# Kernel optimization log

Measured on AMD Instinct MI355X. Metric: run time of the kernel, lower is better.

## Reference

```python
import jax, jax.numpy as jnp
import numpy as np

DT_MIN, DT_MAX = 1e-3, 0.1
DT_RANK, D_STATE = 64, 16


def setup_inputs() -> dict:
    key = jax.random.key(0)
    ks = jax.random.split(key, 8)
    B, L, D_MODEL, D_INNER = 2, 4096, 1024, 2048
    s = 0.02
    return {
        "x": jax.random.normal(ks[0], (B, L, D_MODEL), jnp.float32),
        "W_in": jax.random.normal(ks[1], (D_MODEL, 2 * D_INNER), jnp.float32) * s,
        "W_xproj": jax.random.normal(ks[2], (D_INNER, DT_RANK + 2 * D_STATE), jnp.float32) * s,
        "W_dt": jax.random.normal(ks[3], (DT_RANK, D_INNER), jnp.float32) * s,
        "b_dt": jax.random.normal(ks[4], (D_INNER,), jnp.float32) * s,
        "A_log": jnp.log(jax.random.uniform(ks[5], (D_INNER, D_STATE), jnp.float32) + 0.5),
        "D": jnp.ones((D_INNER,), jnp.float32),
        "W_out": jax.random.normal(ks[6], (D_INNER, D_MODEL), jnp.float32) * s,
    }


def _selective_scan(xp, delta, A, Bm, Cm):
    # xp, delta: [B, L, d_inner]; Bm, Cm: [B, L, d_state]; A: [d_inner, d_state]
    batch, L, d_inner = xp.shape
    d_state = A.shape[1]

    def step(h, inp):
        x_t, dt_t, B_t, C_t = inp  # [B,di], [B,di], [B,ds], [B,ds]
        A_bar = 1.0 + A[None] * dt_t[..., None]            # [B, di, ds]
        B_bar = B_t[:, None, :] * dt_t[..., None]          # [B, di, ds]
        h = A_bar * h + B_bar * x_t[..., None]             # [B, di, ds]
        y_t = jnp.sum(C_t[:, None, :] * h, axis=-1)        # [B, di]
        return h, y_t

    h0 = jnp.zeros((batch, d_inner, d_state), xp.dtype)
    xs = (
        jnp.swapaxes(xp, 0, 1),
        jnp.swapaxes(delta, 0, 1),
        jnp.swapaxes(Bm, 0, 1),
        jnp.swapaxes(Cm, 0, 1),
    )
    _, ys = jax.lax.scan(step, h0, xs)  # ys: [L, B, d_inner]
    return jnp.swapaxes(ys, 0, 1)


def reference(x, W_in, W_xproj, W_dt, b_dt, A_log, D, W_out):
    xz = x @ W_in
    xp, z = jnp.split(xz, 2, axis=-1)                      # [B,L,d_inner] each
    x_dbl = xp @ W_xproj
    dlt, Bm, Cm = jnp.split(x_dbl, [DT_RANK, DT_RANK + D_STATE], axis=-1)
    delta = jnp.clip(jax.nn.softplus(dlt @ W_dt + b_dt), DT_MIN, DT_MAX)
    A = -jnp.exp(A_log)
    y = _selective_scan(xp, delta, A, Bm, Cm)
    y = y + D[None, None, :] * xp
    y = y * jax.nn.silu(z)
    return y @ W_out
```

## Files before the change

kernel.cpp:

```cpp
#include <hip/hip_runtime.h>
#include <cstdint>
#include <cstddef>

typedef unsigned short u16;
typedef __attribute__((ext_vector_type(8))) short bf16x8;
typedef __attribute__((ext_vector_type(4))) float f32x4;

__device__ __forceinline__ float bf2f(u16 u) {
  unsigned v = ((unsigned)u) << 16;
  return __builtin_bit_cast(float, v);
}
__device__ __forceinline__ u16 f2bf(float f) {
  unsigned u = __builtin_bit_cast(unsigned, f);
  u = (u + 0x7FFFu + ((u >> 16) & 1u)) >> 16;
  return (u16)u;
}

__device__ __forceinline__ void gload16(const void* g, void* l) {
  __builtin_amdgcn_global_load_lds(
      (const __attribute__((address_space(1))) void*)g,
      (__attribute__((address_space(3))) void*)l,
      16, 0, 0);
}

__device__ __forceinline__ int swz(int lb) { return lb ^ (((lb >> 7) & 7) << 4); }

__global__ __launch_bounds__(256) void f32_to_bf16_kernel(
    const float* __restrict__ in, u16* __restrict__ out, int n) {
  int i = (blockIdx.x * 256 + threadIdx.x) * 4;
  if (i < n) {
    float4 v = *(const float4*)(in + i);
    ushort4 o;
    o.x = f2bf(v.x); o.y = f2bf(v.y); o.z = f2bf(v.z); o.w = f2bf(v.w);
    *(ushort4*)(out + i) = o;
  }
}

__global__ void transpose_f32_bf16T_kernel(
    const float* __restrict__ in, u16* __restrict__ out, int R, int C) {
  __shared__ float tile[32][33];
  const int bx = blockIdx.x * 32;
  const int by = blockIdx.y * 32;
  const int tx = threadIdx.x, ty = threadIdx.y;
#pragma unroll
  for (int i = 0; i < 32; i += 8)
    tile[ty + i][tx] = in[(size_t)(by + ty + i) * C + bx + tx];
  __syncthreads();
#pragma unroll
  for (int i = 0; i < 32; i += 8)
    out[(size_t)(bx + ty + i) * R + by + tx] = f2bf(tile[tx][ty + i]);
}

template <int BN, int EPI>
__global__ __launch_bounds__(512, 2) void gemm256(
    const u16* __restrict__ Ap, const u16* __restrict__ Btp,
    int M, int N, int K, int gx,
    void* __restrict__ o0, void* __restrict__ o1) {
  constexpr int NFR = BN / 64;
  constexpr int NFH = NFR / 2;
  constexpr int B_ISS = BN / 64;
  constexpr int BH = B_ISS / 2;
  constexpr int WN = BN / 4;
  constexpr int HSH = (BN == 256) ? 5 : 4;
  constexpr int AREG = 32768;
  constexpr int BREG = BN * 128;
  __shared__ __align__(1024) char smem[AREG + BREG];

  const int tid = threadIdx.x;
  const int wid = tid >> 6, lane = tid & 63;
  const int wr = wid >> 2, wc = wid & 3;
  const int l16 = lane & 15, lk = lane >> 4;

  const int nwg = gridDim.x, bid = blockIdx.x;
  const int rb = (bid & 7) * (nwg >> 3) + (bid >> 3);
  const int bx = rb % gx, by = rb / gx;
  const int m0 = by * 256, n0 = bx * BN;

  const u16* gA[4];
  const u16* gB[B_ISS];
#pragma unroll
  for (int i = 0; i < 4; ++i) {
    int lb = swz(i * 8192 + tid * 16);
    gA[i] = Ap + (size_t)(m0 + (lb >> 7)) * K + ((lb & 127) >> 1);
  }
#pragma unroll
  for (int i = 0; i < B_ISS; ++i) {
    int lb = swz(i * 8192 + tid * 16);
    int rl = lb >> 7;
    int half = (rl >= BN / 2) ? 1 : 0;
    int r = rl & (BN / 2 - 1);
    int n = ((r >> HSH) << (HSH + 1)) + (half << HSH) + (r & ((1 << HSH) - 1));
    gB[i] = Btp + (size_t)(n0 + n) * K + ((lb & 127) >> 1);
  }

  auto stageA = [&](int kt, int h) {
    char* dst = smem + (wid << 10);
    gload16(gA[h] + kt * 64, dst + h * 8192);
    gload16(gA[h + 2] + kt * 64, dst + (h + 2) * 8192);
  };
  auto stageB = [&](int kt, int h) {
    char* dst = smem + AREG + (wid << 10);
#pragma unroll
    for (int j = 0; j < BH; ++j)
      gload16(gB[h * BH + j] + kt * 64, dst + (h * BH + j) * 8192);
  };

  auto offA = [&](int f, int kk) {
    return swz((wr * 128 + f * 16 + l16) * 128 + kk * 64 + lk * 16);
  };
  auto offB = [&](int nf, int kk) {
    int rl = (nf >= NFH ? BN / 2 : 0) + wc * (WN / 2) + (nf % NFH) * 16 + l16;
    return swz(rl * 128 + kk * 64 + lk * 16);
  };

  f32x4 acc[8][NFR];
#pragma unroll
  for (int f = 0; f < 8; ++f)
#pragma unroll
    for (int n = 0; n < NFR; ++n) {
      f32x4 z = {0.f, 0.f, 0.f, 0.f};
      acc[f][n] = z;
    }

  const char* bufA = smem;
  const char* bufB = smem + AREG;
  const int NT = K >> 6;
  stageA(0, 0); stageB(0, 0); stageB(0, 1); stageA(0, 1);
  if constexpr (BH == 2) asm volatile("s_waitcnt vmcnt(4)" ::: "memory");
  else                   asm volatile("s_waitcnt vmcnt(3)" ::: "memory");
  __builtin_amdgcn_s_barrier();

  for (int kt = 0; kt < NT; ++kt) {
    bf16x8 af[4][2], bh[2][NFH][2];

#pragma unroll
    for (int j = 0; j < 4; ++j)
#pragma unroll
      for (int kk = 0; kk < 2; ++kk)
        af[j][kk] = *(const bf16x8*)(bufA + offA(j, kk));
#pragma unroll
    for (int j = 0; j < NFH; ++j)
#pragma unroll
      for (int kk = 0; kk < 2; ++kk)
        bh[0][j][kk] = *(const bf16x8*)(bufB + offB(j, kk));
    __builtin_amdgcn_s_barrier();
    asm volatile("s_waitcnt lgkmcnt(0)" ::: "memory");
    __builtin_amdgcn_sched_barrier(0);
    __builtin_amdgcn_s_setprio(1);
#pragma unroll
    for (int j = 0; j < 4; ++j)
#pragma unroll
      for (int n2 = 0; n2 < NFH; ++n2)
#pragma unroll
        for (int kk = 0; kk < 2; ++kk)
          acc[j][n2] = __builtin_amdgcn_mfma_f32_16x16x32_bf16(
              af[j][kk], bh[0][n2][kk], acc[j][n2], 0, 0, 0);
    __builtin_amdgcn_s_setprio(0);
    asm volatile("s_waitcnt vmcnt(2)" ::: "memory");
    __builtin_amdgcn_s_barrier();

#pragma unroll
    for (int j = 0; j < NFH; ++j)
#pragma unroll
      for (int kk = 0; kk < 2; ++kk)
        bh[1][j][kk] = *(const bf16x8*)(bufB + offB(NFH + j, kk));
    if (kt + 1 < NT) { stageA(kt + 1, 0); stageB(kt + 1, 0); }
    __builtin_amdgcn_s_barrier();
    asm volatile("s_waitcnt lgkmcnt(0)" ::: "memory");
    __builtin_amdgcn_sched_barrier(0);
    __builtin_amdgcn_s_setprio(1);
#pragma unroll
    for (int j = 0; j < 4; ++j)
#pragma unroll
      for (int n2 = 0; n2 < NFH; ++n2)
#pragma unroll
        for (int kk = 0; kk < 2; ++kk)
          acc[j][NFH + n2] = __builtin_amdgcn_mfma_f32_16x16x32_bf16(
              af[j][kk], bh[1][n2][kk], acc[j][NFH + n2], 0, 0, 0);
    __builtin_amdgcn_s_setprio(0);
    if (kt + 1 < NT) {
      if constexpr (BH == 2) asm volatile("s_waitcnt vmcnt(4)" ::: "memory");
      else                   asm volatile("s_waitcnt vmcnt(3)" ::: "memory");
    } else {
      asm volatile("s_waitcnt vmcnt(0)" ::: "memory");
    }
    __builtin_amdgcn_s_barrier();

#pragma unroll
    for (int j = 0; j < 4; ++j)
#pragma unroll
      for (int kk = 0; kk < 2; ++kk)
        af[j][kk] = *(const bf16x8*)(bufA + offA(4 + j, kk));
    if (kt + 1 < NT) stageB(kt + 1, 1);
    __builtin_amdgcn_s_barrier();
    asm volatile("s_waitcnt lgkmcnt(0)" ::: "memory");
    __builtin_amdgcn_sched_barrier(0);
    __builtin_amdgcn_s_setprio(1);
#pragma unroll
    for (int j = 0; j < 4; ++j)
#pragma unroll
      for (int n2 = 0; n2 < NFH; ++n2)
#pragma unroll
        for (int kk = 0; kk < 2; ++kk)
          acc[4 + j][NFH + n2] = __builtin_amdgcn_mfma_f32_16x16x32_bf16(
              af[j][kk], bh[1][n2][kk], acc[4 + j][NFH + n2], 0, 0, 0);
    __builtin_amdgcn_s_setprio(0);
    __builtin_amdgcn_s_barrier();

    if (kt + 1 < NT) stageA(kt + 1, 1);
    __builtin_amdgcn_s_setprio(1);
#pragma unroll
    for (int j = 0; j < 4; ++j)
#pragma unroll
      for (int n2 = 0; n2 < NFH; ++n2)
#pragma unroll
        for (int kk = 0; kk < 2; ++kk)
          acc[4 + j][n2] = __builtin_amdgcn_mfma_f32_16x16x32_bf16(
              af[j][kk], bh[0][n2][kk], acc[4 + j][n2], 0, 0, 0);
    __builtin_amdgcn_s_setprio(0);
    if (kt + 1 < NT) {
      if constexpr (BH == 2) asm volatile("s_waitcnt vmcnt(4)" ::: "memory");
      else                   asm volatile("s_waitcnt vmcnt(3)" ::: "memory");
    }
    __builtin_amdgcn_s_barrier();
  }

#pragma unroll
  for (int f = 0; f < 8; ++f) {
#pragma unroll
    for (int n = 0; n < NFR; ++n) {
#pragma unroll
      for (int rr = 0; rr < 4; ++rr) {
        const int row = m0 + wr * 128 + f * 16 + lk * 4 + rr;
        const int col = n0 + wc * WN + n * 16 + l16;
        float v = acc[f][n][rr];
        if constexpr (EPI == 0) {
          if (col < 2048) {
            ((u16*)o0)[(size_t)row * 2048 + col] = f2bf(v);
          } else {
            float sv = v / (1.f + __expf(-v));
            ((u16*)o1)[(size_t)row * 2048 + (col - 2048)] = f2bf(sv);
          }
        } else {
          ((float*)o0)[(size_t)row * (size_t)N + col] = v;
        }
      }
    }
  }
}

template <int BN, int NR, int EPI>
__global__ __launch_bounds__(256) void gemm_bt(
    const u16* __restrict__ A, const u16* __restrict__ Bt,
    int M, int N, int K, int KS,
    void* __restrict__ o0, const float* __restrict__ bias) {
  constexpr int BM = 128, BK = 32, MR = 4;
  __shared__ __align__(16) u16 As[BM * BK];
  __shared__ __align__(16) u16 Bs[BN * BK];
  const int tid = threadIdx.x;
  const int wid = tid >> 6, lane = tid & 63;
  const int wr = wid >> 1, wc = wid & 1;
  const int m0 = blockIdx.y * BM, n0 = blockIdx.x * BN;
  const int l16 = lane & 15, lk = lane >> 4;

  f32x4 acc[MR][NR];
#pragma unroll
  for (int m = 0; m < MR; ++m)
#pragma unroll
    for (int n = 0; n < NR; ++n) {
      f32x4 z = {0.f, 0.f, 0.f, 0.f};
      acc[m][n] = z;
    }

  constexpr int CH_A = (BM * BK * 2) / 1024;
  constexpr int CH_B = (BN * BK * 2) / 1024;

  const int kbeg = blockIdx.z * KS, kend = kbeg + KS;
  for (int k0 = kbeg; k0 < kend; k0 += BK) {
    for (int c = wid; c < CH_A; c += 4) {
      int off = c * 1024 + lane * 16;
      int e = off >> 1;
      int m = e >> 5, kk = e & 31;
      gload16(A + (size_t)(m0 + m) * K + (k0 + kk), (char*)As + off);
    }
    for (int c = wid; c < CH_B; c += 4) {
      int off = c * 1024 + lane * 16;
      int e = off >> 1;
      int n = e >> 5, kk = e & 31;
      gload16(Bt + (size_t)(n0 + n) * K + (k0 + kk), (char*)Bs + off);
    }
    __syncthreads();
    bf16x8 af[MR], bfr[NR];
#pragma unroll
    for (int m = 0; m < MR; ++m)
      af[m] = *(const bf16x8*)(As + (wr * 64 + m * 16 + l16) * BK + lk * 8);
#pragma unroll
    for (int n = 0; n < NR; ++n)
      bfr[n] = *(const bf16x8*)(Bs + (wc * (NR * 16) + n * 16 + l16) * BK + lk * 8);
#pragma unroll
    for (int m = 0; m < MR; ++m)
#pragma unroll
      for (int n = 0; n < NR; ++n)
        acc[m][n] = __builtin_amdgcn_mfma_f32_16x16x32_bf16(af[m], bfr[n], acc[m][n], 0, 0, 0);
    __syncthreads();
  }

#pragma unroll
  for (int m = 0; m < MR; ++m) {
#pragma unroll
    for (int n = 0; n < NR; ++n) {
#pragma unroll
      for (int r = 0; r < 4; ++r) {
        const int row = m0 + wr * 64 + m * 16 + (lane >> 4) * 4 + r;
        const int col = n0 + wc * (NR * 16) + n * 16 + (lane & 15);
        float v = acc[m][n][r];
        if constexpr (EPI == 2) {
          v += bias[col];
          float sp = (v > 20.f) ? v : log1pf(__expf(v));
          sp = fminf(fmaxf(sp, 1e-3f), 0.1f);
          ((u16*)o0)[(size_t)row * 2048 + col] = f2bf(sp);
        } else {
          ((float*)o0)[((size_t)blockIdx.z * M + row) * 96 + col] = v;
        }
      }
    }
  }
}

__global__ __launch_bounds__(256) void reduce_xdbl(
    const float* __restrict__ part, u16* __restrict__ dlt,
    float* __restrict__ Bc, float* __restrict__ Cc) {
  int idx = blockIdx.x * 256 + threadIdx.x;
  int row = idx / 24, c4 = idx % 24;
  const float* p = part + (size_t)row * 96 + c4 * 4;
  f32x4 v = *(const f32x4*)p;
#pragma unroll
  for (int z = 1; z < 4; ++z)
    v += *(const f32x4*)(p + (size_t)z * 8192 * 96);
  int col = c4 * 4;
  if (col < 64) {
    ushort4 o;
    o.x = f2bf(v[0]); o.y = f2bf(v[1]); o.z = f2bf(v[2]); o.w = f2bf(v[3]);
    *(ushort4*)(dlt + (size_t)row * 64 + col) = o;
  } else if (col < 80) {
    *(f32x4*)(Bc + (size_t)row * 16 + (col - 64)) = v;
  } else {
    *(f32x4*)(Cc + (size_t)row * 16 + (col - 80)) = v;
  }
}

template <int TC>
__global__ __launch_bounds__(256) void scan_pass1(
    const u16* __restrict__ xp, const u16* __restrict__ dt,
    const float* __restrict__ Bc, const float* __restrict__ A_log,
    float* __restrict__ P, float* __restrict__ Q, int NC) {
  const int di = blockIdx.x * 256 + threadIdx.x;
  const int c = blockIdx.y, b = blockIdx.z;
  __shared__ __align__(16) float Bs[TC * 16];
  {
    const float* src = Bc + (size_t)(b * 4096 + c * TC) * 16;
    for (int i = threadIdx.x; i < TC * 4; i += 256)
      *(float4*)(Bs + i * 4) = *(const float4*)(src + i * 4);
  }
  float A[16], h[16], Pp[16];
#pragma unroll
  for (int s = 0; s < 16; ++s) {
    A[s] = -__expf(A_log[di * 16 + s]);
    h[s] = 0.f;
    Pp[s] = 1.f;
  }
  __syncthreads();
  size_t gidx = (size_t)(b * 4096 + c * TC) * 2048 + di;
  for (int t = 0; t < TC; ++t, gidx += 2048) {
    float xv = bf2f(xp[gidx]), dv = bf2f(dt[gidx]);
    float dvx = dv * xv;
#pragma unroll
    for (int q = 0; q < 4; ++q) {
      f32x4 bv = ((const f32x4*)(Bs + t * 16))[q];
#pragma unroll
      for (int j = 0; j < 4; ++j) {
        int s = q * 4 + j;
        float abar = fmaf(A[s], dv, 1.f);
        h[s] = fmaf(abar, h[s], bv[j] * dvx);
        Pp[s] *= abar;
      }
    }
  }
  const size_t obase = ((size_t)(b * NC + c) * 16) * 2048 + di;
#pragma unroll
  for (int s = 0; s < 16; ++s) {
    P[obase + (size_t)s * 2048] = Pp[s];
    Q[obase + (size_t)s * 2048] = h[s];
  }
}

__global__ __launch_bounds__(256) void scan_pass2(
    const float* __restrict__ P, const float* __restrict__ Q,
    float* __restrict__ Hin, int NC) {
  const int di = blockIdx.x * 256 + threadIdx.x;
  const int s = blockIdx.y, b = blockIdx.z;
  float hin = 0.f;
  const size_t idx0 = ((size_t)(b * NC) * 16 + s) * 2048 + di;
#pragma unroll 8
  for (int c = 0; c < NC; ++c) {
    size_t idx = idx0 + (size_t)c * (16 * 2048);
    Hin[idx] = hin;
    hin = fmaf(P[idx], hin, Q[idx]);
  }
}

template <int TC>
__global__ __launch_bounds__(256) void scan_pass3(
    const u16* __restrict__ xp, const u16* __restrict__ dt,
    const u16* __restrict__ zs, const float* __restrict__ Bc,
    const float* __restrict__ Cc, const float* __restrict__ A_log,
    const float* __restrict__ Dv, const float* __restrict__ Hin,
    u16* __restrict__ Y, int NC) {
  const int di = blockIdx.x * 256 + threadIdx.x;
  const int c = blockIdx.y, b = blockIdx.z;
  __shared__ __align__(16) float Bs[TC * 16], Cs[TC * 16];
  {
    const float* srcB = Bc + (size_t)(b * 4096 + c * TC) * 16;
    const float* srcC = Cc + (size_t)(b * 4096 + c * TC) * 16;
    for (int i = threadIdx.x; i < TC * 4; i += 256) {
      *(float4*)(Bs + i * 4) = *(const float4*)(srcB + i * 4);
      *(float4*)(Cs + i * 4) = *(const float4*)(srcC + i * 4);
    }
  }
  float A[16], h[16];
  const size_t hbase = ((size_t)(b * NC + c) * 16) * 2048 + di;
#pragma unroll
  for (int s = 0; s < 16; ++s) {
    A[s] = -__expf(A_log[di * 16 + s]);
    h[s] = Hin[hbase + (size_t)s * 2048];
  }
  const float Dg = Dv[di];
  __syncthreads();
  size_t gidx = (size_t)(b * 4096 + c * TC) * 2048 + di;
  for (int t = 0; t < TC; ++t, gidx += 2048) {
    float xv = bf2f(xp[gidx]), dv = bf2f(dt[gidx]), zv = bf2f(zs[gidx]);
    float dvx = dv * xv;
    float y = 0.f;
#pragma unroll
    for (int q = 0; q < 4; ++q) {
      f32x4 bv = ((const f32x4*)(Bs + t * 16))[q];
      f32x4 cv = ((const f32x4*)(Cs + t * 16))[q];
#pragma unroll
      for (int j = 0; j < 4; ++j) {
        int s = q * 4 + j;
        float abar = fmaf(A[s], dv, 1.f);
        h[s] = fmaf(abar, h[s], bv[j] * dvx);
        y = fmaf(cv[j], h[s], y);
      }
    }
    float yo = fmaf(Dg, xv, y) * zv;
    Y[gidx] = f2bf(yo);
  }
}

extern "C" void kernel_launch(void* const* d_in, const int* in_sizes, int n_in,
                              void* d_out, int out_size, void* d_ws, size_t ws_size,
                              hipStream_t stream) {
  (void)in_sizes; (void)n_in; (void)out_size; (void)ws_size;
  const float* x       = (const float*)d_in[0];
  const float* W_in    = (const float*)d_in[1];
  const float* W_xproj = (const float*)d_in[2];
  const float* W_dt    = (const float*)d_in[3];
  const float* b_dt    = (const float*)d_in[4];
  const float* A_log   = (const float*)d_in[5];
  const float* Dv      = (const float*)d_in[6];
  const float* W_out   = (const float*)d_in[7];
  float* out = (float*)d_out;

  constexpr size_t MB = 1ull << 20;
  char* ws = (char*)d_ws;
  constexpr size_t O_XP    = 0;
  constexpr size_t O_ZS    = 32 * MB;
  constexpr size_t O_DELTA = 64 * MB;
  constexpr size_t O_BC    = 96 * MB;
  constexpr size_t O_CC    = O_BC + 512 * 1024;
  constexpr size_t O_WOUTT = 97 * MB;
  constexpr size_t O_Y     = 101 * MB;
  constexpr size_t O_XB    = 133 * MB;
  constexpr size_t O_WINT  = 149 * MB;
  constexpr size_t O_WXT   = 157 * MB;
  constexpr size_t O_WDTT  = O_WXT + 393216;
  constexpr size_t O_DLT   = O_WDTT + 262144;
  constexpr size_t O_P     = 133 * MB;
  constexpr size_t O_Q     = 149 * MB;
  constexpr size_t O_HIN   = 165 * MB;
  constexpr size_t O_XDP   = O_P;

  u16* xb    = (u16*)(ws + O_XB);
  u16* WinT  = (u16*)(ws + O_WINT);
  u16* WxT   = (u16*)(ws + O_WXT);
  u16* WdtT  = (u16*)(ws + O_WDTT);
  u16* WoutT = (u16*)(ws + O_WOUTT);
  u16* xpb   = (u16*)(ws + O_XP);
  u16* zsb   = (u16*)(ws + O_ZS);
  u16* dltb  = (u16*)(ws + O_DLT);
  float* Bcf = (float*)(ws + O_BC);
  float* Ccf = (float*)(ws + O_CC);
  u16* delb  = (u16*)(ws + O_DELTA);
  u16* Yb    = (u16*)(ws + O_Y);
  float* Pf  = (float*)(ws + O_P);
  float* Qf  = (float*)(ws + O_Q);
  float* Hin = (float*)(ws + O_HIN);
  float* xdp = (float*)(ws + O_XDP);

  dim3 tb(32, 8);
  f32_to_bf16_kernel<<<8192 * 1024 / 1024, 256, 0, stream>>>(x, xb, 8192 * 1024);
  transpose_f32_bf16T_kernel<<<dim3(4096 / 32, 1024 / 32), tb, 0, stream>>>(W_in, WinT, 1024, 4096);
  transpose_f32_bf16T_kernel<<<dim3(96 / 32, 2048 / 32), tb, 0, stream>>>(W_xproj, WxT, 2048, 96);
  transpose_f32_bf16T_kernel<<<dim3(2048 / 32, 64 / 32), tb, 0, stream>>>(W_dt, WdtT, 64, 2048);
  transpose_f32_bf16T_kernel<<<dim3(1024 / 32, 2048 / 32), tb, 0, stream>>>(W_out, WoutT, 2048, 1024);

  gemm256<256, 0><<<512, 512, 0, stream>>>(
      xb, WinT, 8192, 4096, 1024, 16, xpb, zsb);
  gemm_bt<96, 3, 4><<<dim3(1, 8192 / 128, 4), 256, 0, stream>>>(
      xpb, WxT, 8192, 96, 2048, 512, xdp, nullptr);
  reduce_xdbl<<<8192 * 24 / 256, 256, 0, stream>>>(xdp, dltb, Bcf, Ccf);
  gemm_bt<128, 4, 2><<<dim3(2048 / 128, 8192 / 128, 1), 256, 0, stream>>>(
      dltb, WdtT, 8192, 2048, 64, 64, delb, b_dt);

  constexpr int NC = 64, TC = 64;
  scan_pass1<TC><<<dim3(8, NC, 2), 256, 0, stream>>>(
      xpb, delb, Bcf, A_log, Pf, Qf, NC);
  scan_pass2<<<dim3(8, 16, 2), 256, 0, stream>>>(Pf, Qf, Hin, NC);
  scan_pass3<TC><<<dim3(8, NC, 2), 256, 0, stream>>>(
      xpb, delb, zsb, Bcf, Ccf, A_log, Dv, Hin, Yb, NC);

  gemm256<128, 3><<<256, 512, 0, stream>>>(
      Yb, WoutT, 8192, 1024, 2048, 8, out, nullptr);
}
```

Before: 322.6 us.

## Split-K the output projection GEMM into two slices with a reduction kernel

Adds a K-slice parameter to the 256-row GEMM so the output projection runs with a grid of two K-halves, each writing fp32 partials into dead workspace. A new vectorized kernel sums the two partials into the output. The aim is to double the block count of the output GEMM to fill the CUs better, at the cost of extra partial write/read traffic and an additional launch.

```diff
diff --git a/kernel.cpp b/kernel.cpp
--- a/kernel.cpp
+++ b/kernel.cpp
@@ -54,7 +54,7 @@
 template <int BN, int EPI>
 __global__ __launch_bounds__(512, 2) void gemm256(
     const u16* __restrict__ Ap, const u16* __restrict__ Btp,
-    int M, int N, int K, int gx,
+    int M, int N, int K, int gx, int ksl,
     void* __restrict__ o0, void* __restrict__ o1) {
   constexpr int NFR = BN / 64;
   constexpr int NFH = NFR / 2;
@@ -75,13 +75,14 @@
   const int rb = (bid & 7) * (nwg >> 3) + (bid >> 3);
   const int bx = rb % gx, by = rb / gx;
   const int m0 = by * 256, n0 = bx * BN;
+  const int kbase = blockIdx.z * ksl;
 
   const u16* gA[4];
   const u16* gB[B_ISS];
 #pragma unroll
   for (int i = 0; i < 4; ++i) {
     int lb = swz(i * 8192 + tid * 16);
-    gA[i] = Ap + (size_t)(m0 + (lb >> 7)) * K + ((lb & 127) >> 1);
+    gA[i] = Ap + (size_t)(m0 + (lb >> 7)) * K + kbase + ((lb & 127) >> 1);
   }
 #pragma unroll
   for (int i = 0; i < B_ISS; ++i) {
@@ -90,7 +91,7 @@
     int half = (rl >= BN / 2) ? 1 : 0;
     int r = rl & (BN / 2 - 1);
     int n = ((r >> HSH) << (HSH + 1)) + (half << HSH) + (r & ((1 << HSH) - 1));
-    gB[i] = Btp + (size_t)(n0 + n) * K + ((lb & 127) >> 1);
+    gB[i] = Btp + (size_t)(n0 + n) * K + kbase + ((lb & 127) >> 1);
   }
 
   auto stageA = [&](int kt, int h) {
@@ -124,7 +125,7 @@
 
   const char* bufA = smem;
   const char* bufB = smem + AREG;
-  const int NT = K >> 6;
+  const int NT = ksl >> 6;
   stageA(0, 0); stageB(0, 0); stageB(0, 1); stageA(0, 1);
   if constexpr (BH == 2) asm volatile("s_waitcnt vmcnt(4)" ::: "memory");
   else                   asm volatile("s_waitcnt vmcnt(3)" ::: "memory");
@@ -242,10 +243,20 @@
             ((u16*)o1)[(size_t)row * 2048 + (col - 2048)] = f2bf(sv);
           }
         } else {
-          ((float*)o0)[(size_t)row * (size_t)N + col] = v;
+          ((float*)o0)[(size_t)blockIdx.z * M * N + (size_t)row * N + col] = v;
         }
       }
     }
+  }
+}
+
+__global__ __launch_bounds__(256) void reduce_out(
+    const float* __restrict__ part, float* __restrict__ out, int n) {
+  int i = (blockIdx.x * 256 + threadIdx.x) * 4;
+  if (i < n) {
+    f32x4 v = *(const f32x4*)(part + i);
+    v += *(const f32x4*)(part + (size_t)n + i);
+    *(f32x4*)(out + i) = v;
   }
 }
 
@@ -490,6 +501,7 @@
   constexpr size_t O_Q     = 149 * MB;
   constexpr size_t O_HIN   = 165 * MB;
   constexpr size_t O_XDP   = O_P;
+  constexpr size_t O_ODP   = 0;
 
   u16* xb    = (u16*)(ws + O_XB);
   u16* WinT  = (u16*)(ws + O_WINT);
@@ -507,6 +519,7 @@
   float* Qf  = (float*)(ws + O_Q);
   float* Hin = (float*)(ws + O_HIN);
   float* xdp = (float*)(ws + O_XDP);
+  float* odp = (float*)(ws + O_ODP);
 
   dim3 tb(32, 8);
   f32_to_bf16_kernel<<<8192 * 1024 / 1024, 256, 0, stream>>>(x, xb, 8192 * 1024);
@@ -515,8 +528,8 @@
   transpose_f32_bf16T_kernel<<<dim3(2048 / 32, 64 / 32), tb, 0, stream>>>(W_dt, WdtT, 64, 2048);
   transpose_f32_bf16T_kernel<<<dim3(1024 / 32, 2048 / 32), tb, 0, stream>>>(W_out, WoutT, 2048, 1024);
 
-  gemm256<256, 0><<<512, 512, 0, stream>>>(
-      xb, WinT, 8192, 4096, 1024, 16, xpb, zsb);
+  gemm256<256, 0><<<dim3(512, 1, 1), 512, 0, stream>>>(
+      xb, WinT, 8192, 4096, 1024, 16, 1024, xpb, zsb);
   gemm_bt<96, 3, 4><<<dim3(1, 8192 / 128, 4), 256, 0, stream>>>(
       xpb, WxT, 8192, 96, 2048, 512, xdp, nullptr);
   reduce_xdbl<<<8192 * 24 / 256, 256, 0, stream>>>(xdp, dltb, Bcf, Ccf);
@@ -530,6 +543,7 @@
   scan_pass3<TC><<<dim3(8, NC, 2), 256, 0, stream>>>(
       xpb, delb, zsb, Bcf, Ccf, A_log, Dv, Hin, Yb, NC);
 
-  gemm256<128, 3><<<256, 512, 0, stream>>>(
-      Yb, WoutT, 8192, 1024, 2048, 8, out, nullptr);
-}
+  gemm256<128, 5><<<dim3(256, 1, 2), 512, 0, stream>>>(
+      Yb, WoutT, 8192, 1024, 2048, 8, 1024, odp, nullptr);
+  reduce_out<<<8192 * 1024 / 1024, 256, 0, stream>>>(odp, out, 8192 * 1024);
+}
```

After: 348.1 us. 1.08x slower.

## Double GEMM K-tile to 128 with wider swizzled LDS rows and split k-halves

Applied to the files above, without the earlier changes.

The bf16 MFMA GEMM now stages a 128-wide K slice per iteration instead of 64. LDS rows become 256 bytes with a matching XOR swizzle, and each iteration runs two k-half compute passes, with global staging issued only during the second. This halves the number of outer iterations and the barrier/waitcnt overhead per unit of K. Global addressing also switches from 64-bit pointers to 32-bit offsets to save registers. The cost is double the shared memory per block, which likely lowers the blocks per CU allowed by the launch bounds, and waitcnt bookkeeping that is more fragile.

```diff
diff --git a/kernel.cpp b/kernel.cpp
--- a/kernel.cpp
+++ b/kernel.cpp
@@ -23,7 +23,7 @@
       16, 0, 0);
 }
 
-__device__ __forceinline__ int swz(int lb) { return lb ^ (((lb >> 7) & 7) << 4); }
+__device__ __forceinline__ int swzA(int lb) { return lb ^ (((lb >> 8) & 7) << 4); }
 
 __global__ __launch_bounds__(256) void f32_to_bf16_kernel(
     const float* __restrict__ in, u16* __restrict__ out, int n) {
@@ -58,13 +58,11 @@
     void* __restrict__ o0, void* __restrict__ o1) {
   constexpr int NFR = BN / 64;
   constexpr int NFH = NFR / 2;
-  constexpr int B_ISS = BN / 64;
-  constexpr int BH = B_ISS / 2;
   constexpr int WN = BN / 4;
   constexpr int HSH = (BN == 256) ? 5 : 4;
-  constexpr int AREG = 32768;
-  constexpr int BREG = BN * 128;
-  __shared__ __align__(1024) char smem[AREG + BREG];
+  constexpr int NBU = BN / 32;
+  constexpr int AREG = 65536;
+  __shared__ __align__(1024) char smem[AREG + BN * 256];
 
   const int tid = threadIdx.x;
   const int wid = tid >> 6, lane = tid & 63;
@@ -76,41 +74,44 @@
   const int bx = rb % gx, by = rb / gx;
   const int m0 = by * 256, n0 = bx * BN;
 
-  const u16* gA[4];
-  const u16* gB[B_ISS];
-#pragma unroll
-  for (int i = 0; i < 4; ++i) {
-    int lb = swz(i * 8192 + tid * 16);
-    gA[i] = Ap + (size_t)(m0 + (lb >> 7)) * K + ((lb & 127) >> 1);
-  }
-#pragma unroll
-  for (int i = 0; i < B_ISS; ++i) {
-    int lb = swz(i * 8192 + tid * 16);
-    int rl = lb >> 7;
+  unsigned aoff[8];
+#pragma unroll
+  for (int i = 0; i < 8; ++i) {
+    int lb = swzA(i * 8192 + tid * 16);
+    aoff[i] = (unsigned)(m0 + (lb >> 8)) * K + ((lb & 255) >> 1);
+  }
+  unsigned boff_g[NBU];
+#pragma unroll
+  for (int i = 0; i < NBU; ++i) {
+    int lb = swzA(i * 8192 + tid * 16);
+    int rl = lb >> 8;
     int half = (rl >= BN / 2) ? 1 : 0;
     int r = rl & (BN / 2 - 1);
     int n = ((r >> HSH) << (HSH + 1)) + (half << HSH) + (r & ((1 << HSH) - 1));
-    gB[i] = Btp + (size_t)(n0 + n) * K + ((lb & 127) >> 1);
+    boff_g[i] = (unsigned)(n0 + n) * K + ((lb & 255) >> 1);
   }
 
   auto stageA = [&](int kt, int h) {
-    char* dst = smem + (wid << 10);
-    gload16(gA[h] + kt * 64, dst + h * 8192);
-    gload16(gA[h + 2] + kt * 64, dst + (h + 2) * 8192);
+    const int u0 = h * 2;
+    gload16(Ap + aoff[u0] + kt * 128,     smem + u0 * 8192 + (wid << 10));
+    gload16(Ap + aoff[u0 + 1] + kt * 128, smem + (u0 + 1) * 8192 + (wid << 10));
+    gload16(Ap + aoff[u0 + 4] + kt * 128, smem + (u0 + 4) * 8192 + (wid << 10));
+    gload16(Ap + aoff[u0 + 5] + kt * 128, smem + (u0 + 5) * 8192 + (wid << 10));
   };
   auto stageB = [&](int kt, int h) {
-    char* dst = smem + AREG + (wid << 10);
-#pragma unroll
-    for (int j = 0; j < BH; ++j)
-      gload16(gB[h * BH + j] + kt * 64, dst + (h * BH + j) * 8192);
+#pragma unroll
+    for (int j = 0; j < NBU / 2; ++j) {
+      int u = h * (NBU / 2) + j;
+      gload16(Btp + boff_g[u] + kt * 128, smem + AREG + u * 8192 + (wid << 10));
+    }
   };
 
   auto offA = [&](int f, int kk) {
-    return swz((wr * 128 + f * 16 + l16) * 128 + kk * 64 + lk * 16);
+    return swzA((wr * 128 + f * 16 + l16) * 256 + kk * 64 + lk * 16);
   };
   auto offB = [&](int nf, int kk) {
     int rl = (nf >= NFH ? BN / 2 : 0) + wc * (WN / 2) + (nf % NFH) * 16 + l16;
-    return swz(rl * 128 + kk * 64 + lk * 16);
+    return AREG + swzA(rl * 256 + kk * 64 + lk * 16);
   };
 
   f32x4 acc[8][NFR];
@@ -122,28 +123,25 @@
       acc[f][n] = z;
     }
 
-  const char* bufA = smem;
-  const char* bufB = smem + AREG;
-  const int NT = K >> 6;
+  const int NT = K >> 7;
+
   stageA(0, 0); stageB(0, 0); stageB(0, 1); stageA(0, 1);
-  if constexpr (BH == 2) asm volatile("s_waitcnt vmcnt(4)" ::: "memory");
-  else                   asm volatile("s_waitcnt vmcnt(3)" ::: "memory");
+  if constexpr (BN == 256) asm volatile("s_waitcnt vmcnt(8)" ::: "memory");
+  else                     asm volatile("s_waitcnt vmcnt(6)" ::: "memory");
   __builtin_amdgcn_s_barrier();
 
-  for (int kt = 0; kt < NT; ++kt) {
+  auto khalf = [&](int kt, int kb, bool stg, bool hasnext) {
     bf16x8 af[4][2], bh[2][NFH][2];
-
 #pragma unroll
     for (int j = 0; j < 4; ++j)
 #pragma unroll
-      for (int kk = 0; kk < 2; ++kk)
-        af[j][kk] = *(const bf16x8*)(bufA + offA(j, kk));
+      for (int q = 0; q < 2; ++q)
+        af[j][q] = *(const bf16x8*)(smem + offA(j, kb + q));
 #pragma unroll
     for (int j = 0; j < NFH; ++j)
 #pragma unroll
-      for (int kk = 0; kk < 2; ++kk)
-        bh[0][j][kk] = *(const bf16x8*)(bufB + offB(j, kk));
-    __builtin_amdgcn_s_barrier();
+      for (int q = 0; q < 2; ++q)
+        bh[0][j][q] = *(const bf16x8*)(smem + offB(j, kb + q));
     asm volatile("s_waitcnt lgkmcnt(0)" ::: "memory");
     __builtin_amdgcn_sched_barrier(0);
     __builtin_amdgcn_s_setprio(1);
@@ -152,20 +150,21 @@
 #pragma unroll
       for (int n2 = 0; n2 < NFH; ++n2)
 #pragma unroll
-        for (int kk = 0; kk < 2; ++kk)
+        for (int q = 0; q < 2; ++q)
           acc[j][n2] = __builtin_amdgcn_mfma_f32_16x16x32_bf16(
-              af[j][kk], bh[0][n2][kk], acc[j][n2], 0, 0, 0);
+              af[j][q], bh[0][n2][q], acc[j][n2], 0, 0, 0);
     __builtin_amdgcn_s_setprio(0);
-    asm volatile("s_waitcnt vmcnt(2)" ::: "memory");
+    if (!stg) {
+      asm volatile("s_waitcnt vmcnt(4)" ::: "memory");
+    }
     __builtin_amdgcn_s_barrier();
 
+    if (stg && hasnext) { stageA(kt + 1, 0); stageB(kt + 1, 0); }
 #pragma unroll
     for (int j = 0; j < NFH; ++j)
 #pragma unroll
-      for (int kk = 0; kk < 2; ++kk)
-        bh[1][j][kk] = *(const bf16x8*)(bufB + offB(NFH + j, kk));
-    if (kt + 1 < NT) { stageA(kt + 1, 0); stageB(kt + 1, 0); }
-    __builtin_amdgcn_s_barrier();
+      for (int q = 0; q < 2; ++q)
+        bh[1][j][q] = *(const bf16x8*)(smem + offB(NFH + j, kb + q));
     asm volatile("s_waitcnt lgkmcnt(0)" ::: "memory");
     __builtin_amdgcn_sched_barrier(0);
     __builtin_amdgcn_s_setprio(1);
@@ -174,25 +173,21 @@
 #pragma unroll
       for (int n2 = 0; n2 < NFH; ++n2)
 #pragma unroll
-        for (int kk = 0; kk < 2; ++kk)
+        for (int q = 0; q < 2; ++q)
           acc[j][NFH + n2] = __builtin_amdgcn_mfma_f32_16x16x32_bf16(
-              af[j][kk], bh[1][n2][kk], acc[j][NFH + n2], 0, 0, 0);
+              af[j][q], bh[1][n2][q], acc[j][NFH + n2], 0, 0, 0);
     __builtin_amdgcn_s_setprio(0);
-    if (kt + 1 < NT) {
-      if constexpr (BH == 2) asm volatile("s_waitcnt vmcnt(4)" ::: "memory");
-      else                   asm volatile("s_waitcnt vmcnt(3)" ::: "memory");
-    } else {
+    if (!stg) {
       asm volatile("s_waitcnt vmcnt(0)" ::: "memory");
     }
     __builtin_amdgcn_s_barrier();
 
+    if (stg && hasnext) stageB(kt + 1, 1);
 #pragma unroll
     for (int j = 0; j < 4; ++j)
 #pragma unroll
-      for (int kk = 0; kk < 2; ++kk)
-        af[j][kk] = *(const bf16x8*)(bufA + offA(4 + j, kk));
-    if (kt + 1 < NT) stageB(kt + 1, 1);
-    __builtin_amdgcn_s_barrier();
+      for (int q = 0; q < 2; ++q)
+        af[j][q] = *(const bf16x8*)(smem + offA(4 + j, kb + q));
     asm volatile("s_waitcnt lgkmcnt(0)" ::: "memory");
     __builtin_amdgcn_sched_barrier(0);
     __builtin_amdgcn_s_setprio(1);
@@ -201,28 +196,35 @@
 #pragma unroll
       for (int n2 = 0; n2 < NFH; ++n2)
 #pragma unroll
-        for (int kk = 0; kk < 2; ++kk)
+        for (int q = 0; q < 2; ++q)
           acc[4 + j][NFH + n2] = __builtin_amdgcn_mfma_f32_16x16x32_bf16(
-              af[j][kk], bh[1][n2][kk], acc[4 + j][NFH + n2], 0, 0, 0);
+              af[j][q], bh[1][n2][q], acc[4 + j][NFH + n2], 0, 0, 0);
     __builtin_amdgcn_s_setprio(0);
-    __builtin_amdgcn_s_barrier();
-
-    if (kt + 1 < NT) stageA(kt + 1, 1);
+    if (stg) __builtin_amdgcn_s_barrier();
+
+    if (stg && hasnext) stageA(kt + 1, 1);
     __builtin_amdgcn_s_setprio(1);
 #pragma unroll
     for (int j = 0; j < 4; ++j)
 #pragma unroll
       for (int n2 = 0; n2 < NFH; ++n2)
 #pragma unroll
-        for (int kk = 0; kk < 2; ++kk)
+        for (int q = 0; q < 2; ++q)
           acc[4 + j][n2] = __builtin_amdgcn_mfma_f32_16x16x32_bf16(
-              af[j][kk], bh[0][n2][kk], acc[4 + j][n2], 0, 0, 0);
+              af[j][q], bh[0][n2][q], acc[4 + j][n2], 0, 0, 0);
     __builtin_amdgcn_s_setprio(0);
-    if (kt + 1 < NT) {
-      if constexpr (BH == 2) asm volatile("s_waitcnt vmcnt(4)" ::: "memory");
-      else                   asm volatile("s_waitcnt vmcnt(3)" ::: "memory");
-    }
-    __builtin_amdgcn_s_barrier();
+    if (stg) {
+      if (hasnext) {
+        if constexpr (BN == 256) asm volatile("s_waitcnt vmcnt(8)" ::: "memory");
+        else                     asm volatile("s_waitcnt vmcnt(6)" ::: "memory");
+      }
+      __builtin_amdgcn_s_barrier();
+    }
+  };
+
+  for (int kt = 0; kt < NT; ++kt) {
+    khalf(kt, 0, false, false);
+    khalf(kt, 2, true, kt + 1 < NT);
   }
 
 #pragma unroll
```

Result: slower. 363.8 us (+12.8%).
